# Optimization experiments

Measured on AMD Instinct MI355X. Metric: run time of the kernel, lower is better.

## Reference

```python
import jax, jax.numpy as jnp
import numpy as np

TWO_PI = 2.0 * np.pi


def _fftfreq(n, d):
    # numpy-compatible fftfreq, trace/grad-safe in d: [0..n/2-1, -n/2..-1]/(n*d)
    k = jnp.arange(n)
    k = jnp.where(k < (n + 1) // 2, k, k - n).astype(jnp.float32)
    return k / (n * d)


def _forward(x, wp1_re, wp1_im, wp2_re, wp2_im, wr_re, wr_im, ty, tx):
    wp1 = (wp1_re + 1j * wp1_im).astype(jnp.complex64)   # [Ci,Co,m1]
    wp2 = (wp2_re + 1j * wp2_im).astype(jnp.complex64)   # [Ci,Co,m2]
    wr = (wr_re + 1j * wr_im).astype(jnp.complex64)      # [Ci,Co,m1,m2]
    Ny, Nx = x.shape[-2], x.shape[-1]
    dty = ty[1] - ty[0]
    dtx = tx[1] - tx[0]

    alpha = jnp.fft.fft2(x, axes=(-2, -1))               # [B,Ci,Ny,Nx] complex
    lam1 = (1j * TWO_PI * _fftfreq(Ny, dty)).astype(jnp.complex64)  # [Ny]
    lam2 = (1j * TWO_PI * _fftfreq(Nx, dtx)).astype(jnp.complex64)  # [Nx]

    # Pole-residue transfer function factors: Hw = wr / ((lam1-p1)(lam2-p2))
    A1 = 1.0 / (lam1 - wp1[..., None])                   # [Ci,Co,m1,Ny]
    A2 = 1.0 / (lam2 - wp2[..., None])                   # [Ci,Co,m2,Nx]

    # sum over poles (p,q) of Hw -> [Ci,Co,Ny,Nx]
    Hsum = jnp.einsum('ikpq,ikpo,ikqx->ikox', wr, A1, A2)
    res1 = jnp.einsum('biox,ikox->bkox', alpha, Hsum)    # [B,Co,Ny,Nx]
    # sum over frequency grid (o,x) -> residue coefficients [B,Co,m1,m2]
    res2 = jnp.einsum('biox,ikpq,ikpo,ikqx->bkpq', alpha, wr, A1, A2)

    x1 = jnp.real(jnp.fft.ifft2(res1, s=(Ny, Nx), axes=(-2, -1)))

    # explicit pole-exponential evaluation over the spatial grid
    E1 = jnp.exp(wp1[..., None] * ty.astype(jnp.complex64))  # [Ci,Co,m1,Ny]
    E2 = jnp.exp(wp2[..., None] * tx.astype(jnp.complex64))  # [Ci,Co,m2,Nx]
    # res2 channel dim contracts against E1/E2's first (in==out required)
    x2 = jnp.real(jnp.einsum('kbpq,bipz,biqx->kizx', res2, E1, E2)) / (Nx * Ny)
    return x1 + x2


def setup_inputs() -> dict:
    key = jax.random.key(0)
    B, Ci, Co, Ny, Nx, m1, m2 = 8, 32, 32, 128, 128, 4, 5
    ks = jax.random.split(key, 7)
    scale = 1.0 / (Ci * Co)
    x = jax.random.normal(ks[0], (B, Ci, Ny, Nx), jnp.float32)
    wp1_re = scale * jax.random.uniform(ks[1], (Ci, Co, m1), jnp.float32)
    wp1_im = scale * jax.random.uniform(ks[2], (Ci, Co, m1), jnp.float32)
    wp2_re = scale * jax.random.uniform(ks[3], (Ci, Co, m2), jnp.float32)
    wp2_im = scale * jax.random.uniform(ks[4], (Ci, Co, m2), jnp.float32)
    wr_re = scale * jax.random.uniform(ks[5], (Ci, Co, m1, m2), jnp.float32)
    wr_im = scale * jax.random.uniform(ks[6], (Ci, Co, m1, m2), jnp.float32)
    ty = (jnp.arange(Ny) / Ny).astype(jnp.float32)
    tx = (jnp.arange(Nx) / Nx).astype(jnp.float32)
    return dict(x=x, wp1_re=wp1_re, wp1_im=wp1_im, wp2_re=wp2_re, wp2_im=wp2_im,
                wr_re=wr_re, wr_im=wr_im, ty=ty, tx=tx)


def reference(x, wp1_re, wp1_im, wp2_re, wp2_im, wr_re, wr_im, ty, tx):
    return _forward(x, wp1_re, wp1_im, wp2_re, wp2_im, wr_re, wr_im, ty, tx)
```

## Files before the change

kernel.cpp:

```cpp
#include <hip/hip_runtime.h>
#include <math.h>

#define N 128
#define B 8
#define CI 32
#define CO 32
#define M1 4
#define M2 5
#define IK (CI*CO)
#define IKP (IK*M1)
#define IKQ (IK*M2)
#define TWO_PI_F 6.2831853071795864769f

__device__ __forceinline__ float2 cmul(float2 a, float2 b){
    return make_float2(fmaf(a.x,b.x,-(a.y*b.y)), fmaf(a.x,b.y,a.y*b.x));
}
__device__ __forceinline__ float2 cmadd(float2 acc, float2 a, float2 b){
    acc.x = fmaf(a.x, b.x, fmaf(-a.y, b.y, acc.x));
    acc.y = fmaf(a.x, b.y, fmaf( a.y, b.x, acc.y));
    return acc;
}

__global__ void k_A1T(const float* wr_, const float* wi_, const float* t_, float2* A1T){
    int idx = blockIdx.x*256 + threadIdx.x;
    int o   = idx >> 12;
    int ikp = idx & (IKP-1);
    float d = t_[1]-t_[0];
    float invnd = 1.0f/((float)N*d);
    int kk = (o < N/2) ? o : o - N;
    float lam = TWO_PI_F * (float)kk * invnd;
    float dr = -wr_[ikp];
    float di = lam - wi_[ikp];
    float inv = 1.0f/(dr*dr + di*di);
    A1T[idx] = make_float2(dr*inv, -di*inv);
}

__global__ void k_A2(const float* wr_, const float* wi_, const float* t_, float2* A2){
    int idx = blockIdx.x*256 + threadIdx.x;
    int ikq = idx >> 7; int xx = idx & (N-1);
    float d = t_[1]-t_[0];
    float invnd = 1.0f/((float)N*d);
    int kk = (xx < N/2) ? xx : xx - N;
    float lam = TWO_PI_F * (float)kk * invnd;
    float dr = -wr_[ikq];
    float di = lam - wi_[ikq];
    float inv = 1.0f/(dr*dr + di*di);
    A2[idx] = make_float2(dr*inv, -di*inv);
}

__global__ void k_E(const float* wr_, const float* wi_, const float* t_, float2* E){
    int idx = blockIdx.x*256 + threadIdx.x;
    int ikp = idx >> 7; int y = idx & (N-1);
    float t = t_[y];
    float m = expf(wr_[ikp]*t);
    float s, c; sincosf(wi_[ikp]*t, &s, &c);
    E[idx] = make_float2(m*c, m*s);
}

__global__ void k_W2N(const float* wrr, const float* wri, const float2* A2, float2* W2N){
    int idx = blockIdx.x*256 + threadIdx.x;
    int ikp = idx >> 7; int xx = idx & (N-1);
    int ik = ikp >> 2; int p = ikp & 3;
    float2 acc = make_float2(0.f,0.f);
    const float* wr0 = wrr + ik*(M1*M2) + p*M2;
    const float* wi0 = wri + ik*(M1*M2) + p*M2;
    const float2* a2 = A2 + (size_t)ik*(M2*N) + xx;
    #pragma unroll
    for(int q=0;q<M2;q++){
        float2 w = make_float2(wr0[q], wi0[q]);
        acc = cmadd(acc, w, a2[q*N]);
    }
    W2N[(size_t)ikp*N + xx] = acc;
}

template<int SIGNPOS, int REALIN, int SCALE>
__global__ void __launch_bounds__(256) k_fft_rows(const void* in_, float2* out){
    const float sgn = SIGNPOS ? 1.0f : -1.0f;
    __shared__ float tre[16*132];
    __shared__ float tim_[16*132];
    __shared__ float zre[16*136];
    __shared__ float zim[16*136];
    __shared__ float twc[128], tws[128];
    int t = threadIdx.x;
    size_t row0 = (size_t)blockIdx.x * 16;

    if(t < 128){ float s,c; sincosf(sgn*(TWO_PI_F/128.f)*(float)t, &s,&c); twc[t]=c; tws[t]=s; }

    if(REALIN){
        const float* src = (const float*)in_ + row0*N;
        #pragma unroll
        for(int j=0;j<8;j++){
            int idx = t + 256*j; int r = idx>>7, cl = idx&127;
            tre[r*132+cl] = src[idx];
        }
    } else {
        const float2* src = (const float2*)in_ + row0*N;
        #pragma unroll
        for(int j=0;j<8;j++){
            int idx = t + 256*j; int r = idx>>7, cl = idx&127;
            float2 v = src[idx];
            tre[r*132+cl] = v.x; tim_[r*132+cl] = v.y;
        }
    }
    __syncthreads();

    float t16c[16], t16s[16];
    #pragma unroll
    for(int j=0;j<16;j++){ t16c[j]=twc[8*j]; t16s[j]=tws[8*j]; }

    int r = t>>4, u = t&15, b = u&7, h = u>>3;
    float xr[16], xi[16];
    #pragma unroll
    for(int a=0;a<16;a++){
        float vr = tre[r*132 + 8*a + b];
        float vi = REALIN ? 0.f : tim_[r*132 + 8*a + b];
        if(h && (a&1)){ vr = -vr; vi = -vi; }
        xr[a]=vr; xi[a]=vi;
    }
    #pragma unroll
    for(int cc=0; cc<8; cc++){
        float yr=0.f, yi=0.f;
        #pragma unroll
        for(int a=0;a<16;a++){
            int j = (a*cc)&15;
            if(REALIN){
                yr = fmaf(xr[a], t16c[j], yr);
                yi = fmaf(xr[a], t16s[j], yi);
            } else {
                yr = fmaf(xr[a], t16c[j], yr); yr = fmaf(-xi[a], t16s[j], yr);
                yi = fmaf(xr[a], t16s[j], yi); yi = fmaf( xi[a], t16c[j], yi);
            }
        }
        int c = 8*h + cc;
        int jw = b*c;
        float co = twc[jw], s = tws[jw];
        zre[r*136 + b*17 + c] = fmaf(yr,co,-(yi*s));
        zim[r*136 + b*17 + c] = fmaf(yr,s,  yi*co);
    }
    __syncthreads();

    float t8c[8], t8s[8];
    #pragma unroll
    for(int j=0;j<8;j++){ t8c[j]=twc[16*j]; t8s[j]=tws[16*j]; }
    int r2 = t>>4, c2 = t&15;
    float zr_[8], zi_[8];
    #pragma unroll
    for(int bb=0;bb<8;bb++){ zr_[bb]=zre[r2*136 + bb*17 + c2]; zi_[bb]=zim[r2*136 + bb*17 + c2]; }
    float2* dst = out + (row0 + r2)*N;
    #pragma unroll
    for(int d=0; d<8; d++){
        float Xr=0.f, Xi=0.f;
        #pragma unroll
        for(int bb=0;bb<8;bb++){
            int j=(bb*d)&7;
            Xr = fmaf(zr_[bb], t8c[j], Xr); Xr = fmaf(-zi_[bb], t8s[j], Xr);
            Xi = fmaf(zr_[bb], t8s[j], Xi); Xi = fmaf( zi_[bb], t8c[j], Xi);
        }
        if(SCALE){ Xr *= (1.f/128.f); Xi *= (1.f/128.f); }
        dst[c2 + 16*d] = make_float2(Xr, Xi);
    }
}

template<int SIGNPOS, int REALOUT, int SCALE>
__global__ void __launch_bounds__(256) k_fft_cols(const float2* in, float2* outc, float* outr){
    const float sgn = SIGNPOS ? 1.0f : -1.0f;
    __shared__ float tre[N*17];
    __shared__ float tim_[N*17];
    __shared__ float zre[8*16*17];
    __shared__ float zim[8*16*17];
    __shared__ float twc[128], tws[128];
    int t = threadIdx.x;
    int img = blockIdx.x >> 3; int x0 = (blockIdx.x & 7)*16;

    if(t < 128){ float s,c; sincosf(sgn*(TWO_PI_F/128.f)*(float)t, &s,&c); twc[t]=c; tws[t]=s; }

    const float2* src = in + (size_t)img*N*N + x0;
    #pragma unroll
    for(int j=0;j<8;j++){
        int idx = t + 256*j; int y = idx>>4, xc = idx&15;
        float2 v = src[y*N + xc];
        tre[y*17+xc]=v.x; tim_[y*17+xc]=v.y;
    }
    __syncthreads();

    float t16c[16], t16s[16];
    #pragma unroll
    for(int j=0;j<16;j++){ t16c[j]=twc[8*j]; t16s[j]=tws[8*j]; }

    int xc = t&15, u = t>>4, b = u&7, h = u>>3;
    float xr[16], xi[16];
    #pragma unroll
    for(int a=0;a<16;a++){
        int y = 8*a + b;
        float vr = tre[y*17+xc];
        float vi = tim_[y*17+xc];
        if(h && (a&1)){ vr = -vr; vi = -vi; }
        xr[a]=vr; xi[a]=vi;
    }
    #pragma unroll
    for(int cc=0; cc<8; cc++){
        float yr=0.f, yi=0.f;
        #pragma unroll
        for(int a=0;a<16;a++){
            int j = (a*cc)&15;
            yr = fmaf(xr[a], t16c[j], yr); yr = fmaf(-xi[a], t16s[j], yr);
            yi = fmaf(xr[a], t16s[j], yi); yi = fmaf( xi[a], t16c[j], yi);
        }
        int c = 8*h + cc;
        int jw = b*c;
        float co = twc[jw], s = tws[jw];
        zre[(b*16 + c)*17 + xc] = fmaf(yr,co,-(yi*s));
        zim[(b*16 + c)*17 + xc] = fmaf(yr,s,  yi*co);
    }
    __syncthreads();

    float t8c[8], t8s[8];
    #pragma unroll
    for(int j=0;j<8;j++){ t8c[j]=twc[16*j]; t8s[j]=tws[16*j]; }
    int c2 = t>>4; int x2 = t&15;
    float zr_[8], zi_[8];
    #pragma unroll
    for(int bb=0;bb<8;bb++){ zr_[bb]=zre[(bb*16 + c2)*17 + x2]; zi_[bb]=zim[(bb*16 + c2)*17 + x2]; }
    #pragma unroll
    for(int d=0; d<8; d++){
        float Xr=0.f, Xi=0.f;
        #pragma unroll
        for(int bb=0;bb<8;bb++){
            int j=(bb*d)&7;
            Xr = fmaf(zr_[bb], t8c[j], Xr); Xr = fmaf(-zi_[bb], t8s[j], Xr);
            Xi = fmaf(zr_[bb], t8s[j], Xi); Xi = fmaf( zi_[bb], t8c[j], Xi);
        }
        int ky = c2 + 16*d;
        if(REALOUT){
            outr[(size_t)img*N*N + ky*N + x0 + x2] = Xr * (SCALE ? (1.f/128.f) : 1.f);
        } else {
            if(SCALE){ Xr *= (1.f/128.f); Xi *= (1.f/128.f); }
            outc[(size_t)img*N*N + ky*N + x0 + x2] = make_float2(Xr, Xi);
        }
    }
}

__global__ void __launch_bounds__(256) k_res1(const float2* alpha, const float2* A1T,
                                              const float2* W2N, float2* res1){
    __shared__ float4 At4[B*CI*8];
    int t = threadIdx.x;
    int o  = blockIdx.x >> 3;
    int x0 = (blockIdx.x & 7) * 16;

    {
        int im0 = t >> 3, xq = t & 7;
        #pragma unroll
        for(int j=0;j<8;j++){
            int im = im0 + 32*j;
            At4[im*8 + xq] = *(const float4*)(alpha + (size_t)im*(N*N) + o*N + x0 + 2*xq);
        }
    }
    __syncthreads();

    int k = t >> 3, xh = t & 7;
    float2 acc[B][2];
    #pragma unroll
    for(int b=0;b<B;b++){ acc[b][0]=make_float2(0.f,0.f); acc[b][1]=make_float2(0.f,0.f); }

    const float2* a1base = A1T + (size_t)o*IKP + k*M1;
    const float2* w2base = W2N + ((size_t)k*M1)*N + x0 + 2*xh;

    #pragma unroll 2
    for(int i=0;i<CI;i++){
        float4 a1a = *(const float4*)(a1base + (size_t)i*128);
        float4 a1b = *(const float4*)(a1base + (size_t)i*128 + 2);
        float2 a1v[M1] = { make_float2(a1a.x,a1a.y), make_float2(a1a.z,a1a.w),
                           make_float2(a1b.x,a1b.y), make_float2(a1b.z,a1b.w) };
        float2 h0 = make_float2(0.f,0.f), h1 = make_float2(0.f,0.f);
        const float2* w2 = w2base + (size_t)i*(128*N);
        #pragma unroll
        for(int p=0;p<M1;p++){
            float4 wv = *(const float4*)(w2 + (size_t)p*N);
            h0 = cmadd(h0, a1v[p], make_float2(wv.x,wv.y));
            h1 = cmadd(h1, a1v[p], make_float2(wv.z,wv.w));
        }
        #pragma unroll
        for(int b=0;b<B;b++){
            float4 av = At4[(b*CI + i)*8 + xh];
            acc[b][0] = cmadd(acc[b][0], make_float2(av.x,av.y), h0);
            acc[b][1] = cmadd(acc[b][1], make_float2(av.z,av.w), h1);
        }
    }

    #pragma unroll
    for(int b=0;b<B;b++){
        float4 v = make_float4(acc[b][0].x, acc[b][0].y, acc[b][1].x, acc[b][1].y);
        *(float4*)(res1 + (size_t)(b*CO + k)*(N*N) + o*N + x0 + 2*xh) = v;
    }
}

__global__ void __launch_bounds__(512, 4) k_S_res2(const float2* alpha, const float2* A2,
                                                   const float2* A1T, float2* part){
    __shared__ float2 tile[64*33];
    __shared__ float2 A2c[160*33];
    int t = threadIdx.x;
    int ol = t & 15;
    int kl = t >> 4;
    int bid = blockIdx.x;
    int oh = bid & 1;
    int i  = (bid >> 1) & (CI-1);
    int b  = bid >> 6;
    int ik = i*CO + kl;
    const float2* asrc = alpha + ((size_t)(b*CI + i))*(N*N) + (size_t)oh*64*N;
    const float2* a2base = A2 + (size_t)i*(CO*M2*N);

    const int txc = t & 31, trow = t >> 5;
    float2 U[4][5];
    #pragma unroll
    for(int oi=0;oi<4;oi++)
        #pragma unroll
        for(int q=0;q<5;q++) U[oi][q] = make_float2(0.f,0.f);

    float2 pre[4];
    #pragma unroll
    for(int j=0;j<4;j++) pre[j] = asrc[(trow + 16*j)*N + txc];

    for(int c=0; c<4; c++){
        __syncthreads();
        #pragma unroll
        for(int j=0;j<4;j++) tile[(trow + 16*j)*33 + txc] = pre[j];
        #pragma unroll
        for(int s=0;s<10;s++){
            int rs = s*16 + trow;
            A2c[rs*33 + txc] = a2base[(size_t)rs*N + c*32 + txc];
        }
        if(c < 3){
            #pragma unroll
            for(int j=0;j<4;j++) pre[j] = asrc[(trow + 16*j)*N + (c+1)*32 + txc];
        }
        __syncthreads();
        #pragma unroll 4
        for(int xc=0; xc<32; xc++){
            float2 a2v[5];
            const float2* a2row = A2c + (kl*5)*33 + xc;
            #pragma unroll
            for(int q=0;q<5;q++) a2v[q] = a2row[q*33];
            #pragma unroll
            for(int oi=0;oi<4;oi++){
                float2 av = tile[(ol + 16*oi)*33 + xc];
                #pragma unroll
                for(int q=0;q<5;q++) U[oi][q] = cmadd(U[oi][q], av, a2v[q]);
            }
        }
    }

    float2 S[4][5];
    #pragma unroll
    for(int p=0;p<4;p++)
        #pragma unroll
        for(int q=0;q<5;q++) S[p][q] = make_float2(0.f,0.f);
    #pragma unroll
    for(int oi=0;oi<4;oi++){
        int o = oh*64 + ol + 16*oi;
        const float2* a1 = A1T + (size_t)o*IKP + (size_t)ik*M1;
        float2 a1v[4];
        #pragma unroll
        for(int p=0;p<4;p++) a1v[p] = a1[p];
        #pragma unroll
        for(int p=0;p<4;p++)
            #pragma unroll
            for(int q=0;q<5;q++) S[p][q] = cmadd(S[p][q], a1v[p], U[oi][q]);
    }
    #pragma unroll
    for(int m=1;m<16;m<<=1){
        #pragma unroll
        for(int p=0;p<4;p++)
            #pragma unroll
            for(int q=0;q<5;q++){
                S[p][q].x += __shfl_xor(S[p][q].x, m);
                S[p][q].y += __shfl_xor(S[p][q].y, m);
            }
    }
    if(ol==0){
        float2* dst = part + ((size_t)((b*CO + kl)*CI + i)*2 + oh)*(M1*M2);
        #pragma unroll
        for(int p=0;p<4;p++)
            #pragma unroll
            for(int q=0;q<5;q++) dst[p*5+q] = S[p][q];
    }
}

__global__ void k_res2_red(const float2* part, const float* wrr, const float* wri, float2* res2){
    int bk = blockIdx.x;
    int t = threadIdx.x;
    int i = t & 31, g = t >> 5;
    int k = bk & (CO-1);
    int ikk = i*CO + k;
    float2 acc[5];
    #pragma unroll
    for(int e=0;e<5;e++){
        int pq = g*5 + e;
        float2 w = make_float2(wrr[ikk*(M1*M2)+pq], wri[ikk*(M1*M2)+pq]);
        const float2* pp = part + ((size_t)(bk*CI + i)*2)*(M1*M2) + pq;
        float2 s0 = pp[0], s1 = pp[M1*M2];
        float2 s = make_float2(s0.x+s1.x, s0.y+s1.y);
        acc[e] = cmul(w, s);
    }
    #pragma unroll
    for(int m=1;m<32;m<<=1){
        #pragma unroll
        for(int e=0;e<5;e++){
            acc[e].x += __shfl_xor(acc[e].x, m);
            acc[e].y += __shfl_xor(acc[e].y, m);
        }
    }
    if(i==0){
        #pragma unroll
        for(int e=0;e<5;e++) res2[(size_t)bk*(M1*M2) + g*5 + e] = acc[e];
    }
}

__global__ void __launch_bounds__(256) k_x2(const float2* res2, const float2* E1,
                                            const float2* E2, float* out){
    __shared__ __align__(16) float2 res2s[CI*M1*M2];
    __shared__ __align__(16) float2 Wt[M1*N];
    __shared__ __align__(16) float2 buf[2][M1*32 + M2*N];
    int t = threadIdx.x;
    int yq = blockIdx.x & 3;
    int j  = (blockIdx.x >> 2) & (CO-1);
    int b  = blockIdx.x >> 7;
    int xt = t & 15, yt = t >> 4;

    {
        const float4* s4 = (const float4*)(res2 + (size_t)b*CO*M1*M2);
        float4* d4 = (float4*)res2s;
        d4[t] = s4[t];
        if(t < 64) d4[256+t] = s4[256+t];
    }

    const bool is1_0 = (t < 64);
    const bool ok1 = (t < 128);
    int off0, dst0;
    if(is1_0){ int pp = t >> 4, rem = (t & 15) << 1; off0 = pp*N + rem; dst0 = pp*32 + rem; }
    else     { int g = t - 64; int qq = g >> 6, xi = (g & 63) << 1; off0 = qq*N + xi; dst0 = 128 + qq*128 + xi; }
    int g1 = t + 192; int qq1 = g1 >> 6, xi1 = (g1 & 63) << 1;
    int off1 = qq1*N + xi1;
    int dst1 = 128 + qq1*128 + xi1;

    const float2* E1c = E1 + ((size_t)j*M1)*N + yq*32;
    const float2* E2c = E2 + ((size_t)j*M2)*N;

    float4 pre0 = *(const float4*)((is1_0 ? E1c : E2c) + off0);
    float4 pre1 = ok1 ? *(const float4*)(E2c + off1) : make_float4(0.f,0.f,0.f,0.f);
    *(float4*)(&buf[0][dst0]) = pre0;
    if(ok1) *(float4*)(&buf[0][dst1]) = pre1;
    int cur = 0;
    __syncthreads();

    float acc[2][8];
    #pragma unroll
    for(int yy=0;yy<2;yy++)
        #pragma unroll
        for(int s=0;s<8;s++) acc[yy][s] = 0.f;

    for(int c=0; c<CI; c++){
        const float2* E2s = buf[cur] + 128;
        #pragma unroll
        for(int s=0;s<2;s++){
            int e = t + 256*s;
            int pp = e >> 7, xi = e & 127;
            const float2* rr = res2s + c*(M1*M2) + pp*M2;
            float2 w = make_float2(0.f,0.f);
            #pragma unroll
            for(int q=0;q<M2;q++) w = cmadd(w, rr[q], E2s[q*128 + xi]);
            Wt[pp*128 + xi] = w;
        }
        if(c+1 < CI){
            E1c += (size_t)CO*M1*N;
            E2c += (size_t)CO*M2*N;
            pre0 = *(const float4*)((is1_0 ? E1c : E2c) + off0);
            if(ok1) pre1 = *(const float4*)(E2c + off1);
        }
        __syncthreads();

        const float2* E1s = buf[cur];
        #pragma unroll
        for(int p=0;p<4;p++){
            float4 a = *(const float4*)(E1s + p*32 + yt*2);
            float2 e0 = make_float2(a.x,a.y);
            float2 e1v = make_float2(a.z,a.w);
            #pragma unroll
            for(int s=0;s<4;s++){
                float4 wv = *(const float4*)(Wt + p*128 + 32*s + 2*xt);
                acc[0][2*s]   = fmaf(e0.x, wv.x, fmaf(-e0.y, wv.y, acc[0][2*s]));
                acc[0][2*s+1] = fmaf(e0.x, wv.z, fmaf(-e0.y, wv.w, acc[0][2*s+1]));
                acc[1][2*s]   = fmaf(e1v.x, wv.x, fmaf(-e1v.y, wv.y, acc[1][2*s]));
                acc[1][2*s+1] = fmaf(e1v.x, wv.z, fmaf(-e1v.y, wv.w, acc[1][2*s+1]));
            }
        }
        if(c+1 < CI){
            float2* nb = buf[cur^1];
            *(float4*)(nb + dst0) = pre0;
            if(ok1) *(float4*)(nb + dst1) = pre1;
        }
        cur ^= 1;
        __syncthreads();
    }

    const float sc = 1.0f/((float)N*(float)N);
    size_t base = (size_t)(b*CO + j)*(N*N) + (size_t)(yq*32)*N;
    #pragma unroll
    for(int yy=0;yy<2;yy++){
        float* orow = out + base + (size_t)(yt*2 + yy)*N;
        #pragma unroll
        for(int s=0;s<4;s++){
            float2* dst = (float2*)(orow + 32*s + 2*xt);
            float2 old = *dst;
            *dst = make_float2(old.x + acc[yy][2*s]*sc, old.y + acc[yy][2*s+1]*sc);
        }
    }
}

extern "C" void kernel_launch(void* const* d_in, const int* in_sizes, int n_in,
                              void* d_out, int out_size, void* d_ws, size_t ws_size,
                              hipStream_t stream){
    const float* x    = (const float*)d_in[0];
    const float* wp1r = (const float*)d_in[1];
    const float* wp1i = (const float*)d_in[2];
    const float* wp2r = (const float*)d_in[3];
    const float* wp2i = (const float*)d_in[4];
    const float* wrr  = (const float*)d_in[5];
    const float* wri  = (const float*)d_in[6];
    const float* ty   = (const float*)d_in[7];
    const float* tx   = (const float*)d_in[8];
    float* out = (float*)d_out;
    float2* ws = (float2*)d_ws;

    const size_t NCIMG = (size_t)B*CI*N*N;
    float2* bufA  = ws;
    float2* alpha = bufA  + NCIMG;
    float2* res1  = alpha + NCIMG;
    float2* A1T   = res1  + NCIMG;
    float2* A2    = A1T   + (size_t)N*IKP;
    float2* W2N   = A2    + (size_t)IKQ*N;
    float2* E1    = W2N   + (size_t)N*IKP;
    float2* E2    = E1    + (size_t)IKP*N;
    float2* res2  = E2    + (size_t)IKQ*N;
    float2* part  = res2  + (size_t)B*CO*M1*M2;

    k_A1T<<<(N*IKP)/256, 256, 0, stream>>>(wp1r, wp1i, ty, A1T);
    k_E  <<<(IKP*N)/256, 256, 0, stream>>>(wp1r, wp1i, ty, E1);
    k_A2 <<<(IKQ*N)/256, 256, 0, stream>>>(wp2r, wp2i, tx, A2);
    k_E  <<<(IKQ*N)/256, 256, 0, stream>>>(wp2r, wp2i, tx, E2);
    k_W2N<<<(IKP*N)/256, 256, 0, stream>>>(wrr, wri, A2, W2N);

    k_fft_rows<0,1,0><<<(B*CI*N)/16, 256, 0, stream>>>((const void*)x, bufA);
    k_fft_cols<0,0,0><<<B*CI*8, 256, 0, stream>>>(bufA, alpha, nullptr);

    k_res1<<<N*8, 256, 0, stream>>>(alpha, A1T, W2N, res1);
    k_S_res2<<<B*CI*2, 512, 0, stream>>>(alpha, A2, A1T, part);
    k_res2_red<<<B*CO, 128, 0, stream>>>(part, wrr, wri, res2);

    k_fft_rows<1,0,1><<<(B*CO*N)/16, 256, 0, stream>>>((const void*)res1, bufA);
    k_fft_cols<1,1,1><<<B*CO*8, 256, 0, stream>>>(bufA, nullptr, out);
    k_x2<<<B*CO*4, 256, 0, stream>>>(res2, E1, E2, out);
}
```

Before: 309.8 us.

## Fuse pole-factor precompute kernels into one launch and prefetch A2 chunks

Merges the five small precompute kernels (A1T, E1, A2, E2, W2N) into a single block-partitioned kernel. W2N now recomputes its A2 factors inline, which removes its dependency on the A2 buffer and lets all parts run concurrently. Separately, the S/res2 kernel now prefetches the next A2 column chunk into registers, so the global loads overlap with compute, as the alpha tile loads already did. The cost is some redundant division work in the W2N path and ten more live registers per thread in the S kernel, which could reduce occupancy.

```diff
diff --git a/kernel.cpp b/kernel.cpp
--- a/kernel.cpp
+++ b/kernel.cpp
@@ -21,56 +21,71 @@
     return acc;
 }
 
-__global__ void k_A1T(const float* wr_, const float* wi_, const float* t_, float2* A1T){
-    int idx = blockIdx.x*256 + threadIdx.x;
-    int o   = idx >> 12;
-    int ikp = idx & (IKP-1);
-    float d = t_[1]-t_[0];
-    float invnd = 1.0f/((float)N*d);
-    int kk = (o < N/2) ? o : o - N;
-    float lam = TWO_PI_F * (float)kk * invnd;
-    float dr = -wr_[ikp];
-    float di = lam - wi_[ikp];
-    float inv = 1.0f/(dr*dr + di*di);
-    A1T[idx] = make_float2(dr*inv, -di*inv);
-}
-
-__global__ void k_A2(const float* wr_, const float* wi_, const float* t_, float2* A2){
-    int idx = blockIdx.x*256 + threadIdx.x;
-    int ikq = idx >> 7; int xx = idx & (N-1);
-    float d = t_[1]-t_[0];
-    float invnd = 1.0f/((float)N*d);
-    int kk = (xx < N/2) ? xx : xx - N;
-    float lam = TWO_PI_F * (float)kk * invnd;
-    float dr = -wr_[ikq];
-    float di = lam - wi_[ikq];
-    float inv = 1.0f/(dr*dr + di*di);
-    A2[idx] = make_float2(dr*inv, -di*inv);
-}
-
-__global__ void k_E(const float* wr_, const float* wi_, const float* t_, float2* E){
-    int idx = blockIdx.x*256 + threadIdx.x;
-    int ikp = idx >> 7; int y = idx & (N-1);
-    float t = t_[y];
-    float m = expf(wr_[ikp]*t);
-    float s, c; sincosf(wi_[ikp]*t, &s, &c);
-    E[idx] = make_float2(m*c, m*s);
-}
-
-__global__ void k_W2N(const float* wrr, const float* wri, const float2* A2, float2* W2N){
-    int idx = blockIdx.x*256 + threadIdx.x;
-    int ikp = idx >> 7; int xx = idx & (N-1);
-    int ik = ikp >> 2; int p = ikp & 3;
-    float2 acc = make_float2(0.f,0.f);
-    const float* wr0 = wrr + ik*(M1*M2) + p*M2;
-    const float* wi0 = wri + ik*(M1*M2) + p*M2;
-    const float2* a2 = A2 + (size_t)ik*(M2*N) + xx;
-    #pragma unroll
-    for(int q=0;q<M2;q++){
-        float2 w = make_float2(wr0[q], wi0[q]);
-        acc = cmadd(acc, w, a2[q*N]);
-    }
-    W2N[(size_t)ikp*N + xx] = acc;
+__global__ void __launch_bounds__(256) k_prep(const float* wp1r, const float* wp1i,
+                                              const float* wp2r, const float* wp2i,
+                                              const float* wrr, const float* wri,
+                                              const float* ty, const float* tx,
+                                              float2* A1T, float2* E1, float2* A2,
+                                              float2* E2, float2* W2N){
+    int bid = blockIdx.x;
+    int t = threadIdx.x;
+    if(bid < 2048){
+        int idx = bid*256 + t;
+        int o   = idx >> 12;
+        int ikp = idx & (IKP-1);
+        float d = ty[1]-ty[0];
+        float invnd = 1.0f/((float)N*d);
+        int kk = (o < N/2) ? o : o - N;
+        float lam = TWO_PI_F * (float)kk * invnd;
+        float dr = -wp1r[ikp];
+        float di = lam - wp1i[ikp];
+        float inv = 1.0f/(dr*dr + di*di);
+        A1T[idx] = make_float2(dr*inv, -di*inv);
+    } else if(bid < 4096){
+        int idx = (bid-2048)*256 + t;
+        int ikp = idx >> 7; int y = idx & (N-1);
+        float tv = ty[y];
+        float m = expf(wp1r[ikp]*tv);
+        float s, c; sincosf(wp1i[ikp]*tv, &s, &c);
+        E1[idx] = make_float2(m*c, m*s);
+    } else if(bid < 6656){
+        int idx = (bid-4096)*256 + t;
+        int ikq = idx >> 7; int xx = idx & (N-1);
+        float d = tx[1]-tx[0];
+        float invnd = 1.0f/((float)N*d);
+        int kk = (xx < N/2) ? xx : xx - N;
+        float lam = TWO_PI_F * (float)kk * invnd;
+        float dr = -wp2r[ikq];
+        float di = lam - wp2i[ikq];
+        float inv = 1.0f/(dr*dr + di*di);
+        A2[idx] = make_float2(dr*inv, -di*inv);
+    } else if(bid < 9216){
+        int idx = (bid-6656)*256 + t;
+        int ikq = idx >> 7; int xx = idx & (N-1);
+        float tv = tx[xx];
+        float m = expf(wp2r[ikq]*tv);
+        float s, c; sincosf(wp2i[ikq]*tv, &s, &c);
+        E2[idx] = make_float2(m*c, m*s);
+    } else {
+        int idx = (bid-9216)*256 + t;
+        int ikp = idx >> 7; int xx = idx & (N-1);
+        int ik = ikp >> 2; int p = ikp & 3;
+        float d = tx[1]-tx[0];
+        float invnd = 1.0f/((float)N*d);
+        int kk = (xx < N/2) ? xx : xx - N;
+        float lam = TWO_PI_F * (float)kk * invnd;
+        float2 acc = make_float2(0.f,0.f);
+        #pragma unroll
+        for(int q=0;q<M2;q++){
+            float dr = -wp2r[ik*M2+q];
+            float di = lam - wp2i[ik*M2+q];
+            float inv = 1.0f/(dr*dr + di*di);
+            float2 a2 = make_float2(dr*inv, -di*inv);
+            float2 w = make_float2(wrr[ik*(M1*M2)+p*M2+q], wri[ik*(M1*M2)+p*M2+q]);
+            acc = cmadd(acc, w, a2);
+        }
+        W2N[(size_t)ikp*N + xx] = acc;
+    }
 }
 
 template<int SIGNPOS, int REALIN, int SCALE>
@@ -316,22 +331,24 @@
         #pragma unroll
         for(int q=0;q<5;q++) U[oi][q] = make_float2(0.f,0.f);
 
-    float2 pre[4];
+    float2 pre[4], a2pre[10];
     #pragma unroll
     for(int j=0;j<4;j++) pre[j] = asrc[(trow + 16*j)*N + txc];
+    #pragma unroll
+    for(int s=0;s<10;s++) a2pre[s] = a2base[(size_t)(s*16 + trow)*N + txc];
 
     for(int c=0; c<4; c++){
         __syncthreads();
         #pragma unroll
         for(int j=0;j<4;j++) tile[(trow + 16*j)*33 + txc] = pre[j];
         #pragma unroll
-        for(int s=0;s<10;s++){
-            int rs = s*16 + trow;
-            A2c[rs*33 + txc] = a2base[(size_t)rs*N + c*32 + txc];
-        }
+        for(int s=0;s<10;s++) A2c[(s*16 + trow)*33 + txc] = a2pre[s];
         if(c < 3){
-            #pragma unroll
-            for(int j=0;j<4;j++) pre[j] = asrc[(trow + 16*j)*N + (c+1)*32 + txc];
+            int x0n = (c+1)*32;
+            #pragma unroll
+            for(int j=0;j<4;j++) pre[j] = asrc[(trow + 16*j)*N + x0n + txc];
+            #pragma unroll
+            for(int s=0;s<10;s++) a2pre[s] = a2base[(size_t)(s*16 + trow)*N + x0n + txc];
         }
         __syncthreads();
         #pragma unroll 4
@@ -543,11 +560,8 @@
     float2* res2  = E2    + (size_t)IKQ*N;
     float2* part  = res2  + (size_t)B*CO*M1*M2;
 
-    k_A1T<<<(N*IKP)/256, 256, 0, stream>>>(wp1r, wp1i, ty, A1T);
-    k_E  <<<(IKP*N)/256, 256, 0, stream>>>(wp1r, wp1i, ty, E1);
-    k_A2 <<<(IKQ*N)/256, 256, 0, stream>>>(wp2r, wp2i, tx, A2);
-    k_E  <<<(IKQ*N)/256, 256, 0, stream>>>(wp2r, wp2i, tx, E2);
-    k_W2N<<<(IKP*N)/256, 256, 0, stream>>>(wrr, wri, A2, W2N);
+    k_prep<<<11264, 256, 0, stream>>>(wp1r, wp1i, wp2r, wp2i, wrr, wri, ty, tx,
+                                      A1T, E1, A2, E2, W2N);
 
     k_fft_rows<0,1,0><<<(B*CI*N)/16, 256, 0, stream>>>((const void*)x, bufA);
     k_fft_cols<0,0,0><<<B*CI*8, 256, 0, stream>>>(bufA, alpha, nullptr);
```

Measured after the change: 314.7 us. Within noise of the previous version (+1.6%).

## Split res2 projection over four row quarters with smaller tiles and fewer registers

Applied to the files above, without the earlier changes.

k_S_res2 now splits each (b,i) image into four 32-row quarters instead of two 64-row halves, doubling the grid to 1024 blocks. It uses 16-column chunks with smaller shared tiles, halves the per-thread U accumulators, and does the A1 reduction in two phases of two poles each. The aim is lower register and LDS use per block so more blocks fit per CU. The A2 chunk is now reloaded twice as often per block, and the reduction kernel sums four partials instead of two.

```diff
diff --git a/kernel.cpp b/kernel.cpp
--- a/kernel.cpp
+++ b/kernel.cpp
@@ -294,94 +294,95 @@
     }
 }
 
-__global__ void __launch_bounds__(512, 4) k_S_res2(const float2* alpha, const float2* A2,
-                                                   const float2* A1T, float2* part){
-    __shared__ float2 tile[64*33];
-    __shared__ float2 A2c[160*33];
+__global__ void __launch_bounds__(512) k_S_res2(const float2* alpha, const float2* A2,
+                                                const float2* A1T, float2* part){
+    __shared__ float2 tile[32*17];
+    __shared__ float2 A2c[160*17];
     int t = threadIdx.x;
     int ol = t & 15;
     int kl = t >> 4;
     int bid = blockIdx.x;
-    int oh = bid & 1;
-    int i  = (bid >> 1) & (CI-1);
-    int b  = bid >> 6;
+    int oq = bid & 3;
+    int i  = (bid >> 2) & (CI-1);
+    int b  = bid >> 7;
     int ik = i*CO + kl;
-    const float2* asrc = alpha + ((size_t)(b*CI + i))*(N*N) + (size_t)oh*64*N;
+    const float2* asrc = alpha + ((size_t)(b*CI + i))*(N*N) + (size_t)oq*32*N;
     const float2* a2base = A2 + (size_t)i*(CO*M2*N);
 
-    const int txc = t & 31, trow = t >> 5;
-    float2 U[4][5];
-    #pragma unroll
-    for(int oi=0;oi<4;oi++)
+    const int txc = t & 15, trow = t >> 4;
+    float2 U[2][5];
+    #pragma unroll
+    for(int oi=0;oi<2;oi++)
         #pragma unroll
         for(int q=0;q<5;q++) U[oi][q] = make_float2(0.f,0.f);
 
-    float2 pre[4];
-    #pragma unroll
-    for(int j=0;j<4;j++) pre[j] = asrc[(trow + 16*j)*N + txc];
-
-    for(int c=0; c<4; c++){
+    float2 pre, a2pre[5];
+    pre = asrc[trow*N + txc];
+    #pragma unroll
+    for(int s=0;s<5;s++) a2pre[s] = a2base[(size_t)(s*32 + trow)*N + txc];
+
+    for(int c=0; c<8; c++){
         __syncthreads();
-        #pragma unroll
-        for(int j=0;j<4;j++) tile[(trow + 16*j)*33 + txc] = pre[j];
-        #pragma unroll
-        for(int s=0;s<10;s++){
-            int rs = s*16 + trow;
-            A2c[rs*33 + txc] = a2base[(size_t)rs*N + c*32 + txc];
-        }
-        if(c < 3){
-            #pragma unroll
-            for(int j=0;j<4;j++) pre[j] = asrc[(trow + 16*j)*N + (c+1)*32 + txc];
+        tile[trow*17 + txc] = pre;
+        #pragma unroll
+        for(int s=0;s<5;s++) A2c[(s*32 + trow)*17 + txc] = a2pre[s];
+        if(c < 7){
+            int x0n = (c+1)*16;
+            pre = asrc[trow*N + x0n + txc];
+            #pragma unroll
+            for(int s=0;s<5;s++) a2pre[s] = a2base[(size_t)(s*32 + trow)*N + x0n + txc];
         }
         __syncthreads();
         #pragma unroll 4
-        for(int xc=0; xc<32; xc++){
+        for(int xc=0; xc<16; xc++){
             float2 a2v[5];
-            const float2* a2row = A2c + (kl*5)*33 + xc;
-            #pragma unroll
-            for(int q=0;q<5;q++) a2v[q] = a2row[q*33];
-            #pragma unroll
-            for(int oi=0;oi<4;oi++){
-                float2 av = tile[(ol + 16*oi)*33 + xc];
+            const float2* a2row = A2c + (kl*5)*17 + xc;
+            #pragma unroll
+            for(int q=0;q<5;q++) a2v[q] = a2row[q*17];
+            #pragma unroll
+            for(int oi=0;oi<2;oi++){
+                float2 av = tile[(ol + 16*oi)*17 + xc];
                 #pragma unroll
                 for(int q=0;q<5;q++) U[oi][q] = cmadd(U[oi][q], av, a2v[q]);
             }
         }
     }
 
-    float2 S[4][5];
-    #pragma unroll
-    for(int p=0;p<4;p++)
-        #pragma unroll
-        for(int q=0;q<5;q++) S[p][q] = make_float2(0.f,0.f);
-    #pragma unroll
-    for(int oi=0;oi<4;oi++){
-        int o = oh*64 + ol + 16*oi;
-        const float2* a1 = A1T + (size_t)o*IKP + (size_t)ik*M1;
-        float2 a1v[4];
-        #pragma unroll
-        for(int p=0;p<4;p++) a1v[p] = a1[p];
-        #pragma unroll
-        for(int p=0;p<4;p++)
-            #pragma unroll
-            for(int q=0;q<5;q++) S[p][q] = cmadd(S[p][q], a1v[p], U[oi][q]);
-    }
-    #pragma unroll
-    for(int m=1;m<16;m<<=1){
-        #pragma unroll
-        for(int p=0;p<4;p++)
+    #pragma unroll
+    for(int ph=0; ph<2; ph++){
+        float2 S[2][5];
+        #pragma unroll
+        for(int pp2=0;pp2<2;pp2++)
+            #pragma unroll
+            for(int q=0;q<5;q++) S[pp2][q] = make_float2(0.f,0.f);
+        #pragma unroll
+        for(int oi=0;oi<2;oi++){
+            int o = oq*32 + ol + 16*oi;
+            const float2* a1 = A1T + (size_t)o*IKP + (size_t)ik*M1 + ph*2;
+            float2 a1v0 = a1[0], a1v1 = a1[1];
             #pragma unroll
             for(int q=0;q<5;q++){
-                S[p][q].x += __shfl_xor(S[p][q].x, m);
-                S[p][q].y += __shfl_xor(S[p][q].y, m);
+                S[0][q] = cmadd(S[0][q], a1v0, U[oi][q]);
+                S[1][q] = cmadd(S[1][q], a1v1, U[oi][q]);
             }
-    }
-    if(ol==0){
-        float2* dst = part + ((size_t)((b*CO + kl)*CI + i)*2 + oh)*(M1*M2);
-        #pragma unroll
-        for(int p=0;p<4;p++)
-            #pragma unroll
-            for(int q=0;q<5;q++) dst[p*5+q] = S[p][q];
+        }
+        #pragma unroll
+        for(int m=1;m<16;m<<=1){
+            #pragma unroll
+            for(int pp2=0;pp2<2;pp2++)
+                #pragma unroll
+                for(int q=0;q<5;q++){
+                    S[pp2][q].x += __shfl_xor(S[pp2][q].x, m);
+                    S[pp2][q].y += __shfl_xor(S[pp2][q].y, m);
+                }
+        }
+        if(ol==0){
+            float2* dst = part + ((size_t)((b*CO + kl)*CI + i)*4 + oq)*(M1*M2) + ph*2*M2;
+            #pragma unroll
+            for(int pp2=0;pp2<2;pp2++)
+                #pragma unroll
+                for(int q=0;q<5;q++) dst[pp2*5+q] = S[pp2][q];
+        }
     }
 }
 
@@ -396,9 +397,9 @@
     for(int e=0;e<5;e++){
         int pq = g*5 + e;
         float2 w = make_float2(wrr[ikk*(M1*M2)+pq], wri[ikk*(M1*M2)+pq]);
-        const float2* pp = part + ((size_t)(bk*CI + i)*2)*(M1*M2) + pq;
-        float2 s0 = pp[0], s1 = pp[M1*M2];
-        float2 s = make_float2(s0.x+s1.x, s0.y+s1.y);
+        const float2* pp = part + ((size_t)(bk*CI + i)*4)*(M1*M2) + pq;
+        float2 s0 = pp[0], s1 = pp[M1*M2], s2 = pp[2*M1*M2], s3 = pp[3*M1*M2];
+        float2 s = make_float2(s0.x+s1.x+s2.x+s3.x, s0.y+s1.y+s2.y+s3.y);
         acc[e] = cmul(w, s);
     }
     #pragma unroll
@@ -553,7 +554,7 @@
     k_fft_cols<0,0,0><<<B*CI*8, 256, 0, stream>>>(bufA, alpha, nullptr);
 
     k_res1<<<N*8, 256, 0, stream>>>(alpha, A1T, W2N, res1);
-    k_S_res2<<<B*CI*2, 512, 0, stream>>>(alpha, A2, A1T, part);
+    k_S_res2<<<B*CI*4, 512, 0, stream>>>(alpha, A2, A1T, part);
     k_res2_red<<<B*CO, 128, 0, stream>>>(part, wrr, wri, res2);
 
     k_fft_rows<1,0,1><<<(B*CO*N)/16, 256, 0, stream>>>((const void*)res1, bufA);
```

Result: slower. 330.9 us (+6.8%).
